# Kernel tuning notes

Measured on AMD Instinct MI355X. Metric: run time of the kernel, lower is better.

The kernel has to match this reference:

```python
import jax, jax.numpy as jnp
import numpy as np

D_IN = 1024
D_OUT = 1024
NUM_HEADS = 16
HEAD_DIM = D_OUT // NUM_HEADS


def setup_inputs() -> dict:
    key = jax.random.key(0)
    ks = jax.random.split(key, 6)
    s = 0.02
    return {
        "x": jax.random.normal(ks[0], (4, 2048, D_IN), dtype=jnp.float32),
        "Wq": jax.random.normal(ks[1], (D_IN, D_OUT), dtype=jnp.float32) * s,
        "Wk": jax.random.normal(ks[2], (D_IN, D_OUT), dtype=jnp.float32) * s,
        "Wv": jax.random.normal(ks[3], (D_IN, D_OUT), dtype=jnp.float32) * s,
        "Wo": jax.random.normal(ks[4], (D_OUT, D_OUT), dtype=jnp.float32) * s,
        "bo": jax.random.normal(ks[5], (D_OUT,), dtype=jnp.float32) * s,
    }


def reference(x, Wq, Wk, Wv, Wo, bo):
    B, S, _ = x.shape
    # QKV projections (no bias), split into heads: [B, H, S, Dh]
    def split_heads(t):
        return t.reshape(B, S, NUM_HEADS, HEAD_DIM).transpose(0, 2, 1, 3)

    q = split_heads(x @ Wq)
    k = split_heads(x @ Wk)
    v = split_heads(x @ Wv)

    # causal scores [B, H, S, S]; note: original masks BEFORE scaling,
    # but -inf is scale-invariant so softmax(scores/sqrt(d)) with mask is identical.
    scores = jnp.einsum("bhqd,bhkd->bhqk", q, k) / jnp.sqrt(jnp.asarray(HEAD_DIM, x.dtype))
    causal = jnp.tril(jnp.ones((S, S), dtype=bool))
    scores = jnp.where(causal, scores, -jnp.inf)
    attn = jax.nn.softmax(scores, axis=-1)
    # dropout p=0.0 -> identity
    ctx = jnp.einsum("bhqk,bhkd->bhqd", attn, v)  # [B, H, S, Dh]
    ctx = ctx.transpose(0, 2, 1, 3).reshape(B, S, D_OUT)
    return ctx @ Wo + bo
```

## Files before the change

### kernel.cpp

```cpp
#include <hip/hip_runtime.h>
#include <hip/hip_bf16.h>
#include <math.h>


typedef __attribute__((ext_vector_type(8))) short short8;
typedef __attribute__((ext_vector_type(4))) float f32x4;

#define MFMA_BF16(a, b, c) __builtin_amdgcn_mfma_f32_16x16x32_bf16((a), (b), (c), 0, 0, 0)

__device__ __forceinline__ void gld_lds16(const void* g, void* l) {
  __builtin_amdgcn_global_load_lds((const __attribute__((address_space(1))) void*)g,
                                   (__attribute__((address_space(3))) void*)l, 16, 0, 0);
}

__global__ void prep_kernel(const float* __restrict__ x, __hip_bfloat16* __restrict__ xb,
                            const float* __restrict__ W0, const float* __restrict__ W1,
                            const float* __restrict__ W2, const float* __restrict__ W3,
                            __hip_bfloat16* __restrict__ T0, __hip_bfloat16* __restrict__ T1,
                            __hip_bfloat16* __restrict__ T2, __hip_bfloat16* __restrict__ T3) {
  const int bid = blockIdx.x, tid = threadIdx.x;
  if (bid < 8192) {
    int i = bid * 256 + tid;
    float4 v = ((const float4*)x)[i];
    __align__(8) __hip_bfloat16 tmp[4] = {__float2bfloat16(v.x), __float2bfloat16(v.y),
                                          __float2bfloat16(v.z), __float2bfloat16(v.w)};
    ((ushort4*)xb)[i] = *(const ushort4*)tmp;
  } else {
    int zz = bid - 8192;
    int z = zz >> 10, rem = zz & 1023;
    const float* W = (z == 0) ? W0 : (z == 1) ? W1 : (z == 2) ? W2 : W3;
    __hip_bfloat16* Wt = (z == 0) ? T0 : (z == 1) ? T1 : (z == 2) ? T2 : T3;
    __shared__ float tile[32][33];
    int tx = tid & 31, ty = tid >> 5;
    int n0 = (rem & 31) * 32, k0 = (rem >> 5) * 32;
#pragma unroll
    for (int i = 0; i < 4; ++i)
      tile[ty + i * 8][tx] = W[(size_t)(k0 + ty + i * 8) * 1024 + n0 + tx];
    __syncthreads();
#pragma unroll
    for (int i = 0; i < 4; ++i)
      Wt[(size_t)(n0 + ty + i * 8) * 1024 + k0 + tx] = __float2bfloat16(tile[tx][ty + i * 8]);
  }
}

__global__ __launch_bounds__(256, 2) void gemm_qkv(
    const __hip_bfloat16* __restrict__ A, const __hip_bfloat16* __restrict__ Bt,
    __hip_bfloat16* __restrict__ q, __hip_bfloat16* __restrict__ k,
    __hip_bfloat16* __restrict__ vT) {
  __shared__ __align__(16) __hip_bfloat16 As[128 * 64];
  __shared__ __align__(16) __hip_bfloat16 Bs[128 * 64];
  const int tid = threadIdx.x;
  const int lane = tid & 63, wid = tid >> 6;
  const int quad = lane >> 4, l16 = lane & 15;
  const int part = blockIdx.x >> 3;
  const int n0 = (blockIdx.x & 7) * 128;
  const int gn0 = part * 1024 + n0;
  const int m0 = blockIdx.y * 128;
  const int wm = (wid & 1) * 64, wn = (wid >> 1) * 64;
  const int swz = l16 & 7;

  f32x4 acc[4][4] = {};

  for (int k0 = 0; k0 < 1024; k0 += 64) {
    __syncthreads();
#pragma unroll
    for (int i = 0; i < 4; ++i) {
      int sbase = __builtin_amdgcn_readfirstlane(wid * 256 + i * 64);
      int s = sbase + lane;
      int row = s >> 3;
      int ch = (s & 7) ^ (row & 7);
      gld_lds16(A + (size_t)(m0 + row) * 1024 + k0 + ch * 8, &As[sbase * 8]);
      gld_lds16(Bt + (size_t)(gn0 + row) * 1024 + k0 + ch * 8, &Bs[sbase * 8]);
    }
    __syncthreads();

    short8 af[4][2], bfr[4][2];
#pragma unroll
    for (int t = 0; t < 4; ++t)
#pragma unroll
      for (int kc = 0; kc < 2; ++kc) {
        int chp = (kc * 4 + quad) ^ swz;
        af[t][kc]  = *(const short8*)&As[(wm + t * 16 + l16) * 64 + chp * 8];
        bfr[t][kc] = *(const short8*)&Bs[(wn + t * 16 + l16) * 64 + chp * 8];
      }
#pragma unroll
    for (int kc = 0; kc < 2; ++kc)
#pragma unroll
      for (int mt = 0; mt < 4; ++mt)
#pragma unroll
        for (int nt = 0; nt < 4; ++nt)
          acc[mt][nt] = MFMA_BF16(af[mt][kc], bfr[nt][kc], acc[mt][nt]);
  }

  const float CSCL = 0.18033688011112042f;
  if (part < 2) {
    __hip_bfloat16* C = (part == 0) ? q : k;
    const float scl = (part == 0) ? CSCL : 1.0f;
#pragma unroll
    for (int mt = 0; mt < 4; ++mt)
#pragma unroll
      for (int nt = 0; nt < 4; ++nt) {
        int row = m0 + wm + mt * 16 + quad * 4;
        int col = n0 + wn + nt * 16 + l16;
#pragma unroll
        for (int r = 0; r < 4; ++r)
          C[(size_t)(row + r) * 1024 + col] = __float2bfloat16(acc[mt][nt][r] * scl);
      }
  } else {
#pragma unroll
    for (int mt = 0; mt < 4; ++mt)
#pragma unroll
      for (int nt = 0; nt < 4; ++nt) {
        int row = m0 + wm + mt * 16 + quad * 4;
        int nn = n0 + wn + nt * 16 + l16;
        __align__(8) __hip_bfloat16 p4[4];
#pragma unroll
        for (int r = 0; r < 4; ++r) p4[r] = __float2bfloat16(acc[mt][nt][r]);
        *(ushort4*)(vT + (size_t)nn * 8192 + row) = *(const ushort4*)p4;
      }
  }
}

__global__ __launch_bounds__(256, 2) void gemm_bt_f32out(
    const __hip_bfloat16* __restrict__ A, const __hip_bfloat16* __restrict__ Bt,
    float* __restrict__ C, const float* __restrict__ bias, int M, int N, int K) {
  __shared__ __align__(16) __hip_bfloat16 As[128 * 64];
  __shared__ __align__(16) __hip_bfloat16 Bs[128 * 64];
  const int tid = threadIdx.x;
  const int lane = tid & 63, wid = tid >> 6;
  const int quad = lane >> 4, l16 = lane & 15;
  const int m0 = blockIdx.y * 128, n0 = blockIdx.x * 128;
  const int wm = (wid & 1) * 64, wn = (wid >> 1) * 64;
  const int swz = l16 & 7;

  f32x4 acc[4][4] = {};

  for (int k0 = 0; k0 < K; k0 += 64) {
    __syncthreads();
#pragma unroll
    for (int i = 0; i < 4; ++i) {
      int sbase = __builtin_amdgcn_readfirstlane(wid * 256 + i * 64);
      int s = sbase + lane;
      int row = s >> 3;
      int ch = (s & 7) ^ (row & 7);
      gld_lds16(A + (size_t)(m0 + row) * K + k0 + ch * 8, &As[sbase * 8]);
      gld_lds16(Bt + (size_t)(n0 + row) * K + k0 + ch * 8, &Bs[sbase * 8]);
    }
    __syncthreads();

    short8 af[4][2], bfr[4][2];
#pragma unroll
    for (int t = 0; t < 4; ++t)
#pragma unroll
      for (int kc = 0; kc < 2; ++kc) {
        int chp = (kc * 4 + quad) ^ swz;
        af[t][kc]  = *(const short8*)&As[(wm + t * 16 + l16) * 64 + chp * 8];
        bfr[t][kc] = *(const short8*)&Bs[(wn + t * 16 + l16) * 64 + chp * 8];
      }
#pragma unroll
    for (int kc = 0; kc < 2; ++kc)
#pragma unroll
      for (int mt = 0; mt < 4; ++mt)
#pragma unroll
        for (int nt = 0; nt < 4; ++nt)
          acc[mt][nt] = MFMA_BF16(af[mt][kc], bfr[nt][kc], acc[mt][nt]);
  }

#pragma unroll
  for (int mt = 0; mt < 4; ++mt)
#pragma unroll
    for (int nt = 0; nt < 4; ++nt) {
      int row = m0 + wm + mt * 16 + quad * 4;
      int col = n0 + wn + nt * 16 + l16;
      float b = bias[col];
#pragma unroll
      for (int r = 0; r < 4; ++r)
        C[(size_t)(row + r) * N + col] = acc[mt][nt][r] + b;
    }
}

__global__ __launch_bounds__(256, 4) void attn_kernel(
    const __hip_bfloat16* __restrict__ Q, const __hip_bfloat16* __restrict__ Km,
    const __hip_bfloat16* __restrict__ vT, __hip_bfloat16* __restrict__ ctx) {
  const int bid = blockIdx.x;
  const int xcd = bid & 7, loc = bid >> 3;
  const int grp = xcd * 8 + (loc >> 4);
  const int p = loc & 15;
  const int h = grp & 15, b = grp >> 4;
  const size_t rbase = (size_t)b * 2048;
  const int tid = threadIdx.x, lane = tid & 63, wid = tid >> 6;
  const int quad = lane >> 4, l16 = lane & 15;
  const int sw = l16 & 7;

  __shared__ __align__(16) __hip_bfloat16 Ks[64 * 64];
  __shared__ __align__(16) __hip_bfloat16 Vs[64 * 64];
  __shared__ __align__(16) __hip_bfloat16 Ps[4][16 * 64];

  const float NEG_BIG = -1e30f;

#pragma unroll 1
  for (int sub = 0; sub < 2; ++sub) {
    const int t = sub ? (31 - p) : p;
    const int q0 = t * 64;

    short8 qf[2];
#pragma unroll
    for (int kc = 0; kc < 2; ++kc)
      qf[kc] = *(const short8*)(Q + (rbase + q0 + wid * 16 + l16) * 1024 +
                                h * 64 + kc * 32 + quad * 8);

    f32x4 o[4] = {};
    f32x4 lp = {};

#pragma unroll 1
    for (int kt = 0; kt <= t; ++kt) {
      const int kbase = kt * 64;
      __syncthreads();
#pragma unroll
      for (int i = 0; i < 2; ++i) {
        int sbase = __builtin_amdgcn_readfirstlane(i * 256 + wid * 64);
        int s = sbase + lane;
        int row = s >> 3;
        int lch = (s & 7) ^ (row & 7);
        gld_lds16(Km + (rbase + kbase + row) * 1024 + h * 64 + lch * 8, &Ks[sbase * 8]);
        gld_lds16(vT + (size_t)(h * 64 + row) * 8192 + rbase + kbase + lch * 8,
                  &Vs[sbase * 8]);
      }
      __syncthreads();

      f32x4 sv[4];
#pragma unroll
      for (int nt = 0; nt < 4; ++nt) {
        short8 k0 = *(const short8*)&Ks[(nt * 16 + l16) * 64 + ((quad ^ sw) << 3)];
        short8 k1 = *(const short8*)&Ks[(nt * 16 + l16) * 64 + (((4 + quad) ^ sw) << 3)];
        f32x4 z = {0.f, 0.f, 0.f, 0.f};
        z = MFMA_BF16(qf[0], k0, z);
        z = MFMA_BF16(qf[1], k1, z);
        sv[nt] = z;
      }
      if (kt == t) {
#pragma unroll
        for (int nt = 0; nt < 4; ++nt)
#pragma unroll
          for (int r = 0; r < 4; ++r)
            if (nt * 16 + l16 > wid * 16 + quad * 4 + r) sv[nt][r] = NEG_BIG;
      }
#pragma unroll
      for (int nt = 0; nt < 4; ++nt)
#pragma unroll
        for (int r = 0; r < 4; ++r) {
          float pv = __builtin_amdgcn_exp2f(sv[nt][r]);
          lp[r] += pv;
          int rrow = quad * 4 + r;
          int cph = (nt * 2 + (l16 >> 3)) ^ (rrow & 7);
          Ps[wid][rrow * 64 + cph * 8 + (l16 & 7)] = __float2bfloat16(pv);
        }
      short8 pa0 = *(const short8*)&Ps[wid][l16 * 64 + ((quad ^ sw) << 3)];
      short8 pa1 = *(const short8*)&Ps[wid][l16 * 64 + (((4 + quad) ^ sw) << 3)];
#pragma unroll
      for (int dt = 0; dt < 4; ++dt) {
        short8 v0 = *(const short8*)&Vs[(dt * 16 + l16) * 64 + ((quad ^ sw) << 3)];
        short8 v1 = *(const short8*)&Vs[(dt * 16 + l16) * 64 + (((4 + quad) ^ sw) << 3)];
        o[dt] = MFMA_BF16(pa0, v0, o[dt]);
        o[dt] = MFMA_BF16(pa1, v1, o[dt]);
      }
    }

#pragma unroll
    for (int msk = 1; msk <= 8; msk <<= 1)
#pragma unroll
      for (int r = 0; r < 4; ++r)
        lp[r] += __shfl_xor(lp[r], msk, 64);
    float inv[4];
#pragma unroll
    for (int r = 0; r < 4; ++r) inv[r] = 1.f / lp[r];
#pragma unroll
    for (int dt = 0; dt < 4; ++dt)
#pragma unroll
      for (int r = 0; r < 4; ++r)
        ctx[(rbase + q0 + wid * 16 + quad * 4 + r) * 1024 + h * 64 + dt * 16 + l16] =
            __float2bfloat16(o[dt][r] * inv[r]);
  }
}

extern "C" void kernel_launch(void* const* d_in, const int* in_sizes, int n_in,
                              void* d_out, int out_size, void* d_ws, size_t ws_size,
                              hipStream_t stream) {
  const float* x  = (const float*)d_in[0];
  const float* Wq = (const float*)d_in[1];
  const float* Wk = (const float*)d_in[2];
  const float* Wv = (const float*)d_in[3];
  const float* Wo = (const float*)d_in[4];
  const float* bo = (const float*)d_in[5];
  float* out = (float*)d_out;

  char* ws = (char*)d_ws;
  const size_t MB = 1024ull * 1024ull;
  __hip_bfloat16* q   = (__hip_bfloat16*)(ws);
  __hip_bfloat16* k   = (__hip_bfloat16*)(ws + 16 * MB);
  __hip_bfloat16* vT  = (__hip_bfloat16*)(ws + 32 * MB);
  __hip_bfloat16* woT = (__hip_bfloat16*)(ws + 48 * MB);
  __hip_bfloat16* ctx = q;

  char* outc = (char*)d_out;
  __hip_bfloat16* xb    = (__hip_bfloat16*)(outc);
  __hip_bfloat16* wcatT = (__hip_bfloat16*)(outc + 16 * MB);

  prep_kernel<<<8192 + 4096, 256, 0, stream>>>(
      x, xb, Wq, Wk, Wv, Wo,
      wcatT, wcatT + 1024 * 1024, wcatT + 2048 * 1024, woT);

  gemm_qkv<<<dim3(24, 64), 256, 0, stream>>>(xb, wcatT, q, k, vT);

  attn_kernel<<<1024, 256, 0, stream>>>(q, k, vT, ctx);

  gemm_bt_f32out<<<dim3(8, 64), 256, 0, stream>>>(ctx, woT, out, bo, 8192, 1024, 1024);
}
```

Before: 253.9 us.

## Double-buffer K/V tiles in attention to prefetch the next tile during compute

Splits the K and V shared-memory tiles into two buffers. The first tile is loaded before the key loop, and each iteration issues async global-to-LDS loads for the next tile before computing on the current one. This removes one barrier per iteration and aims to hide global load latency behind the MFMA and softmax work. In exchange, K/V LDS use doubles, which may limit occupancy. The overlap also depends on the compiler not inserting a full vmcnt wait before the LDS reads.

After: 254.4 us. No clear change (+0.2%).

```diff
diff --git a/kernel.cpp b/kernel.cpp
--- a/kernel.cpp
+++ b/kernel.cpp
@@ -192,8 +192,8 @@
   const int quad = lane >> 4, l16 = lane & 15;
   const int sw = l16 & 7;
 
-  __shared__ __align__(16) __hip_bfloat16 Ks[64 * 64];
-  __shared__ __align__(16) __hip_bfloat16 Vs[64 * 64];
+  __shared__ __align__(16) __hip_bfloat16 Ks[2][64 * 64];
+  __shared__ __align__(16) __hip_bfloat16 Vs[2][64 * 64];
   __shared__ __align__(16) __hip_bfloat16 Ps[4][16 * 64];
 
   const float NEG_BIG = -1e30f;
@@ -203,6 +203,17 @@
     const int t = sub ? (31 - p) : p;
     const int q0 = t * 64;
 
+    __syncthreads();
+    {
+#pragma unroll
+      for (int i = 0; i < 2; ++i) {
+        int sbase = __builtin_amdgcn_readfirstlane(i * 256 + wid * 64);
+        int s = sbase + lane, row = s >> 3, lch = (s & 7) ^ (row & 7);
+        gld_lds16(Km + (rbase + row) * 1024 + h * 64 + lch * 8, &Ks[0][sbase * 8]);
+        gld_lds16(vT + (size_t)(h * 64 + row) * 8192 + rbase + lch * 8, &Vs[0][sbase * 8]);
+      }
+    }
+
     short8 qf[2];
 #pragma unroll
     for (int kc = 0; kc < 2; ++kc)
@@ -214,25 +225,28 @@
 
 #pragma unroll 1
     for (int kt = 0; kt <= t; ++kt) {
-      const int kbase = kt * 64;
+      const int cur = kt & 1;
       __syncthreads();
-#pragma unroll
-      for (int i = 0; i < 2; ++i) {
-        int sbase = __builtin_amdgcn_readfirstlane(i * 256 + wid * 64);
-        int s = sbase + lane;
-        int row = s >> 3;
-        int lch = (s & 7) ^ (row & 7);
-        gld_lds16(Km + (rbase + kbase + row) * 1024 + h * 64 + lch * 8, &Ks[sbase * 8]);
-        gld_lds16(vT + (size_t)(h * 64 + row) * 8192 + rbase + kbase + lch * 8,
-                  &Vs[sbase * 8]);
-      }
-      __syncthreads();
+      if (kt < t) {
+        const int kb = (kt + 1) * 64;
+#pragma unroll
+        for (int i = 0; i < 2; ++i) {
+          int sbase = __builtin_amdgcn_readfirstlane(i * 256 + wid * 64);
+          int s = sbase + lane, row = s >> 3, lch = (s & 7) ^ (row & 7);
+          gld_lds16(Km + (rbase + kb + row) * 1024 + h * 64 + lch * 8,
+                    &Ks[cur ^ 1][sbase * 8]);
+          gld_lds16(vT + (size_t)(h * 64 + row) * 8192 + rbase + kb + lch * 8,
+                    &Vs[cur ^ 1][sbase * 8]);
+        }
+      }
+      const __hip_bfloat16* Kb = &Ks[cur][0];
+      const __hip_bfloat16* Vb = &Vs[cur][0];
 
       f32x4 sv[4];
 #pragma unroll
       for (int nt = 0; nt < 4; ++nt) {
-        short8 k0 = *(const short8*)&Ks[(nt * 16 + l16) * 64 + ((quad ^ sw) << 3)];
-        short8 k1 = *(const short8*)&Ks[(nt * 16 + l16) * 64 + (((4 + quad) ^ sw) << 3)];
+        short8 k0 = *(const short8*)&Kb[(nt * 16 + l16) * 64 + ((quad ^ sw) << 3)];
+        short8 k1 = *(const short8*)&Kb[(nt * 16 + l16) * 64 + (((4 + quad) ^ sw) << 3)];
         f32x4 z = {0.f, 0.f, 0.f, 0.f};
         z = MFMA_BF16(qf[0], k0, z);
         z = MFMA_BF16(qf[1], k1, z);
@@ -259,8 +273,8 @@
       short8 pa1 = *(const short8*)&Ps[wid][l16 * 64 + (((4 + quad) ^ sw) << 3)];
 #pragma unroll
       for (int dt = 0; dt < 4; ++dt) {
-        short8 v0 = *(const short8*)&Vs[(dt * 16 + l16) * 64 + ((quad ^ sw) << 3)];
-        short8 v1 = *(const short8*)&Vs[(dt * 16 + l16) * 64 + (((4 + quad) ^ sw) << 3)];
+        short8 v0 = *(const short8*)&Vb[(dt * 16 + l16) * 64 + ((quad ^ sw) << 3)];
+        short8 v1 = *(const short8*)&Vb[(dt * 16 + l16) * 64 + (((4 + quad) ^ sw) << 3)];
         o[dt] = MFMA_BF16(pa0, v0, o[dt]);
         o[dt] = MFMA_BF16(pa1, v1, o[dt]);
       }
```
